# Optimization experiments

Hardware: AMD Instinct MI355X
Metric: run time of the kernel (lower is better)

The kernel has to match this reference:

```python
import jax, jax.numpy as jnp
import numpy as np

NUM_HEADS = 16


def setup_inputs() -> dict:
    key = jax.random.key(0)
    ks = jax.random.split(key, 7)
    B, S, D = 2, 2048, 1024
    scale = 1.0 / np.sqrt(D)
    return {
        "queries": jax.random.normal(ks[0], (B, S, D), jnp.float32),
        "keys": jax.random.normal(ks[1], (B, S, D), jnp.float32),
        "values": jax.random.normal(ks[2], (B, S, D), jnp.float32),
        "Wq": jax.random.normal(ks[3], (D, D), jnp.float32) * scale,
        "Wk": jax.random.normal(ks[4], (D, D), jnp.float32) * scale,
        "Wv": jax.random.normal(ks[5], (D, D), jnp.float32) * scale,
        "Wo": jax.random.normal(ks[6], (D, D), jnp.float32) * scale,
    }


def _split_heads(x, h):
    # [B, S, D] -> [B, h, S, D/h]
    B, S, D = x.shape
    return x.reshape(B, S, h, D // h).transpose(0, 2, 1, 3)


def reference(queries, keys, values, Wq, Wk, Wv, Wo):
    h = NUM_HEADS
    q = _split_heads(queries @ Wq, h)  # [B, h, S, dh]
    k = _split_heads(keys @ Wk, h)
    v = _split_heads(values @ Wv, h)
    dh = q.shape[-1]
    scores = jnp.einsum("bhqd,bhkd->bhqk", q, k) / jnp.sqrt(jnp.float32(dh))
    attn = jax.nn.softmax(scores, axis=-1)
    y = jnp.einsum("bhqk,bhkd->bhqd", attn, v)  # [B, h, S, dh]
    B, _, S, _ = y.shape
    y = y.transpose(0, 2, 1, 3).reshape(B, S, h * dh)
    return y @ Wo
```

## Files before the change

### kernel.cpp

```cpp
#include <hip/hip_runtime.h>
#include <hip/hip_bf16.h>


typedef __attribute__((ext_vector_type(8))) short bf16x8;
typedef __attribute__((ext_vector_type(4))) float f32x4;
typedef __attribute__((ext_vector_type(16))) float f32x16;
typedef __attribute__((ext_vector_type(4))) unsigned int u32x4;

#define QSCALE 0.18033688011112042f

__device__ __forceinline__ unsigned short f2b(float f) {
    unsigned int u = __float_as_uint(f);
    u += 0x7FFFu + ((u >> 16) & 1u);
    return (unsigned short)(u >> 16);
}

__device__ __forceinline__ unsigned cvt_pk_bf16(float lo, float hi) {
    unsigned r;
    asm("v_cvt_pk_bf16_f32 %0, %1, %2" : "=v"(r) : "v"(lo), "v"(hi));
    return r;
}

__device__ __forceinline__ void gld_lds16(const void* g, void* l) {
    __builtin_amdgcn_global_load_lds(
        (const __attribute__((address_space(1))) unsigned int*)g,
        (__attribute__((address_space(3))) unsigned int*)l, 16, 0, 0);
}

__global__ __launch_bounds__(256) void f32_to_bf16_3(
    const float* __restrict__ i0, const float* __restrict__ i1, const float* __restrict__ i2,
    unsigned short* __restrict__ o0, unsigned short* __restrict__ o1, unsigned short* __restrict__ o2)
{
    const int z = blockIdx.y;
    const float* in = z == 0 ? i0 : (z == 1 ? i1 : i2);
    unsigned short* out = z == 0 ? o0 : (z == 1 ? o1 : o2);
    int i = blockIdx.x * 256 + threadIdx.x;
    float4 v = ((const float4*)in)[i];
    ushort4 o;
    o.x = f2b(v.x); o.y = f2b(v.y); o.z = f2b(v.z); o.w = f2b(v.w);
    ((ushort4*)out)[i] = o;
}

__global__ __launch_bounds__(256) void transpose_w4(
    const float* __restrict__ W0, const float* __restrict__ W1,
    const float* __restrict__ W2, const float* __restrict__ W3,
    unsigned short* __restrict__ O0, unsigned short* __restrict__ O1,
    unsigned short* __restrict__ O2, unsigned short* __restrict__ O3)
{
    __shared__ unsigned short tile[32][33];
    const int z = blockIdx.z;
    const float* in = z == 0 ? W0 : z == 1 ? W1 : z == 2 ? W2 : W3;
    unsigned short* out = z == 0 ? O0 : z == 1 ? O1 : z == 2 ? O2 : O3;
    const int c0 = blockIdx.x * 32, r0 = blockIdx.y * 32;
    const int tx = threadIdx.x, ty = threadIdx.y;
#pragma unroll
    for (int i = 0; i < 4; ++i)
        tile[ty + i * 8][tx] = f2b(in[(size_t)(r0 + ty + i * 8) * 1024 + c0 + tx]);
    __syncthreads();
#pragma unroll
    for (int i = 0; i < 4; ++i)
        out[(size_t)(c0 + ty + i * 8) * 1024 + r0 + tx] = tile[tx][ty + i * 8];
}

template <int BN, int MODE>
__global__ __launch_bounds__(256) void gemm_bt(
    const unsigned short* __restrict__ A0, const unsigned short* __restrict__ A1,
    const unsigned short* __restrict__ A2,
    const unsigned short* __restrict__ B0, const unsigned short* __restrict__ B1,
    const unsigned short* __restrict__ B2,
    void* __restrict__ Cq, void* __restrict__ Ck, void* __restrict__ Cv)
{
    constexpr int K = 1024, N = 1024;
    constexpr int NB = BN / 32;
    __shared__ unsigned short lds_a[2][128 * 32];
    __shared__ unsigned short lds_b[2][BN * 32];
    const int tid = threadIdx.x;
    const int wid = tid >> 6, ln = tid & 15, lg = (tid & 63) >> 4;
    const int z = (MODE == 1) ? blockIdx.z : 0;
    const unsigned short* A = (z == 0) ? A0 : (z == 1) ? A1 : A2;
    const unsigned short* Bt = (z == 0) ? B0 : (z == 1) ? B1 : B2;
    const int m0 = blockIdx.y * 128, n0 = blockIdx.x * BN;
    const int wr = wid >> 1, wc = wid & 1;

    f32x4 acc[4][NB];
#pragma unroll
    for (int m = 0; m < 4; ++m)
#pragma unroll
        for (int n = 0; n < NB; ++n) acc[m][n] = {};

    const unsigned short* ga = A + (size_t)(m0 + (tid >> 2)) * K + (tid & 3) * 8;
    const unsigned short* gb = Bt + (size_t)(n0 + (tid >> 2)) * K + (tid & 3) * 8;

    auto stage = [&](int buf, int k0) {
        gld_lds16(ga + k0, &lds_a[buf][wid * 512]);
        gld_lds16(ga + k0 + 64 * K, &lds_a[buf][wid * 512 + 2048]);
        gld_lds16(gb + k0, &lds_b[buf][wid * 512]);
        if constexpr (BN == 128) gld_lds16(gb + k0 + 64 * K, &lds_b[buf][wid * 512 + 2048]);
    };

    stage(0, 0);
    __syncthreads();

    for (int k0 = 0; k0 < K; k0 += 32) {
        const int buf = (k0 >> 5) & 1;
        if (k0 + 32 < K) stage(buf ^ 1, k0 + 32);

        bf16x8 af[4], bfr[NB];
#pragma unroll
        for (int m = 0; m < 4; ++m)
            af[m] = *(const bf16x8*)&lds_a[buf][(wr * 64 + m * 16 + ln) * 32 + lg * 8];
#pragma unroll
        for (int n = 0; n < NB; ++n)
            bfr[n] = *(const bf16x8*)&lds_b[buf][(wc * (BN / 2) + n * 16 + ln) * 32 + lg * 8];
#pragma unroll
        for (int m = 0; m < 4; ++m)
#pragma unroll
            for (int n = 0; n < NB; ++n)
                acc[m][n] = __builtin_amdgcn_mfma_f32_16x16x32_bf16(af[m], bfr[n], acc[m][n], 0, 0, 0);
        __syncthreads();
    }

    const int gcb = n0 + wc * (BN / 2) + ln;
    const int grb = m0 + wr * 64 + lg * 4;

    if constexpr (MODE == 0) {
        float* C = (float*)Cq;
#pragma unroll
        for (int m = 0; m < 4; ++m)
#pragma unroll
            for (int n = 0; n < NB; ++n)
#pragma unroll
                for (int r = 0; r < 4; ++r)
                    C[(size_t)(grb + m * 16 + r) * N + gcb + n * 16] = acc[m][n][r];
    } else {
        if (z == 0) {
            unsigned short* C = (unsigned short*)Cq;
#pragma unroll
            for (int m = 0; m < 4; ++m)
#pragma unroll
                for (int n = 0; n < NB; ++n)
#pragma unroll
                    for (int r = 0; r < 4; ++r)
                        C[(size_t)(grb + m * 16 + r) * N + gcb + n * 16] =
                            f2b(acc[m][n][r] * QSCALE);
        } else if (z == 1) {
            unsigned short* Kp = (unsigned short*)Ck;
#pragma unroll
            for (int m = 0; m < 4; ++m)
#pragma unroll
                for (int n = 0; n < NB; ++n) {
                    int gr = grb + m * 16, gc = gcb + n * 16;
                    int bq = gr >> 11, kvg = gr & 2047, kvt = kvg >> 6;
                    int h = gc >> 6, d = gc & 63;
                    size_t img = ((size_t)(bq * 16 + h) * 32 + kvt) * 4096;
                    int ks = d >> 4, hib = (d >> 3) & 1, i = d & 7;
                    int kvb = kvg & 63, T = kvb >> 5;
                    size_t base = img + T * 2048 + ks * 512 + hib * 256 + i;
#pragma unroll
                    for (int r = 0; r < 4; ++r)
                        Kp[base + ((kvb & 31) + r) * 8] = f2b(acc[m][n][r]);
                }
        } else {
            unsigned short* Vp = (unsigned short*)Cv;
#pragma unroll
            for (int m = 0; m < 4; ++m)
#pragma unroll
                for (int n = 0; n < NB; ++n) {
                    int gr = grb + m * 16, gc = gcb + n * 16;
                    int bq = gr >> 11, kvg = gr & 2047, kvt = kvg >> 6;
                    int h = gc >> 6, d = gc & 63;
                    size_t img = ((size_t)(bq * 16 + h) * 32 + kvt) * 4096;
                    int kvb = kvg & 63;
                    int T = kvb >> 5, g = (kvb >> 3) & 3, hib = (kvb >> 2) & 1;
                    int kstep = 2 * T + (g >> 1);
                    int dt = d >> 5, ln31 = d & 31;
                    size_t addr = img + dt * 2048 + kstep * 512 + hib * 256 + ln31 * 8 + (g & 1) * 4;
                    uint2 w;
                    w.x = cvt_pk_bf16(acc[m][n][0], acc[m][n][1]);
                    w.y = cvt_pk_bf16(acc[m][n][2], acc[m][n][3]);
                    *(uint2*)(Vp + addr) = w;
                }
        }
    }
}

__global__ __launch_bounds__(128) void attn_kernel(
    const unsigned short* __restrict__ Qp,
    const unsigned short* __restrict__ Kpack,
    const unsigned short* __restrict__ Vpack,
    unsigned short* __restrict__ Y)
{
    __shared__ unsigned short lds_k[2][4096];
    __shared__ unsigned short lds_v[2][4096];
    const int tid = threadIdx.x;
    const int wid = tid >> 6, lane = tid & 63;
    const int q31 = lane & 31, hi = lane >> 5;

    const int logical = (blockIdx.x & 7) * 128 + (blockIdx.x >> 3);
    const int bx = logical & 31, bh = logical >> 5;
    const int b = bh >> 4, h = bh & 15;
    const int tok0 = b * 2048;
    const int qw = bx * 64 + wid * 32;

    const unsigned short* qrow = Qp + (size_t)(tok0 + qw + q31) * 1024 + h * 64 + hi * 8;
    bf16x8 qf[4];
#pragma unroll
    for (int ks = 0; ks < 4; ++ks) qf[ks] = *(const bf16x8*)(qrow + ks * 16);

    const unsigned short* gk = Kpack + (size_t)bh * (32 * 4096);
    const unsigned short* gv = Vpack + (size_t)bh * (32 * 4096);

    float m_run = -1e30f, l_run = 0.f;
    f32x16 o[2] = {{}, {}};

    auto stage = [&](int buf, int kvt) {
#pragma unroll
        for (int c = 0; c < 4; ++c) {
            int m = c * 2 + wid;
            gld_lds16(gk + (size_t)kvt * 4096 + m * 512 + lane * 8, &lds_k[buf][m * 512]);
            gld_lds16(gv + (size_t)kvt * 4096 + m * 512 + lane * 8, &lds_v[buf][m * 512]);
        }
    };

    stage(0, 0);
    __syncthreads();

    for (int kvt = 0; kvt < 32; ++kvt) {
        const int buf = kvt & 1;
        if (kvt < 31) stage(buf ^ 1, kvt + 1);

        f32x16 st[2];
#pragma unroll
        for (int T = 0; T < 2; ++T) {
            f32x16 zacc = {};
#pragma unroll
            for (int ks = 0; ks < 4; ++ks) {
                bf16x8 ka = *(const bf16x8*)&lds_k[buf][T * 2048 + ks * 512 + lane * 8];
                zacc = __builtin_amdgcn_mfma_f32_32x32x16_bf16(ka, qf[ks], zacc, 0, 0, 0);
            }
            st[T] = zacc;
        }

        float pm = st[0][0];
#pragma unroll
        for (int r = 1; r < 16; ++r) pm = fmaxf(pm, st[0][r]);
#pragma unroll
        for (int r = 0; r < 16; ++r) pm = fmaxf(pm, st[1][r]);
        pm = fmaxf(pm, __shfl_xor(pm, 32));
        const float mn = fmaxf(m_run, pm);
        const float alpha = __builtin_amdgcn_exp2f(m_run - mn);
        m_run = mn;

        float rs = 0.f;
        unsigned pk[2][8];
#pragma unroll
        for (int T = 0; T < 2; ++T)
#pragma unroll
            for (int g = 0; g < 4; ++g) {
                float p0 = __builtin_amdgcn_exp2f(st[T][g * 4 + 0] - mn);
                float p1 = __builtin_amdgcn_exp2f(st[T][g * 4 + 1] - mn);
                float p2 = __builtin_amdgcn_exp2f(st[T][g * 4 + 2] - mn);
                float p3 = __builtin_amdgcn_exp2f(st[T][g * 4 + 3] - mn);
                rs += (p0 + p1) + (p2 + p3);
                pk[T][g * 2 + 0] = cvt_pk_bf16(p0, p1);
                pk[T][g * 2 + 1] = cvt_pk_bf16(p2, p3);
            }
        rs += __shfl_xor(rs, 32);
        l_run = l_run * alpha + rs;

#pragma unroll
        for (int r = 0; r < 16; ++r) { o[0][r] *= alpha; o[1][r] *= alpha; }

#pragma unroll
        for (int dt = 0; dt < 2; ++dt)
#pragma unroll
            for (int kstep = 0; kstep < 4; ++kstep) {
                bf16x8 va = *(const bf16x8*)&lds_v[buf][dt * 2048 + kstep * 512 + lane * 8];
                u32x4 w = {pk[kstep >> 1][4 * (kstep & 1) + 0], pk[kstep >> 1][4 * (kstep & 1) + 1],
                           pk[kstep >> 1][4 * (kstep & 1) + 2], pk[kstep >> 1][4 * (kstep & 1) + 3]};
                o[dt] = __builtin_amdgcn_mfma_f32_32x32x16_bf16(
                    va, __builtin_bit_cast(bf16x8, w), o[dt], 0, 0, 0);
            }
        __syncthreads();
    }

    const float inv = __builtin_amdgcn_rcpf(l_run);
    unsigned short* yout = Y + (size_t)(tok0 + qw + q31) * 1024 + h * 64 + hi * 4;
#pragma unroll
    for (int dt = 0; dt < 2; ++dt)
#pragma unroll
        for (int g = 0; g < 4; ++g) {
            uint2 w;
            w.x = cvt_pk_bf16(o[dt][g * 4 + 0] * inv, o[dt][g * 4 + 1] * inv);
            w.y = cvt_pk_bf16(o[dt][g * 4 + 2] * inv, o[dt][g * 4 + 3] * inv);
            *(uint2*)(yout + dt * 32 + g * 8) = w;
        }
}

extern "C" void kernel_launch(void* const* d_in, const int* in_sizes, int n_in,
                              void* d_out, int out_size, void* d_ws, size_t ws_size,
                              hipStream_t stream)
{
    const float* q_f = (const float*)d_in[0];
    const float* k_f = (const float*)d_in[1];
    const float* v_f = (const float*)d_in[2];
    const float* Wq  = (const float*)d_in[3];
    const float* Wk  = (const float*)d_in[4];
    const float* Wv  = (const float*)d_in[5];
    const float* Wo  = (const float*)d_in[6];
    float* out = (float*)d_out;

    const size_t X = (size_t)4096 * 1024;
    const size_t W = (size_t)1024 * 1024;
    unsigned short* ws  = (unsigned short*)d_ws;
    unsigned short* qb  = ws;
    unsigned short* kb  = qb + X;
    unsigned short* vb  = kb + X;
    unsigned short* wqt = vb + X;
    unsigned short* wkt = wqt + W;
    unsigned short* wvt = wkt + W;
    unsigned short* wot = wvt + W;
    unsigned short* Qp  = wot + W;
    unsigned short* Kpk = Qp + X;
    unsigned short* Vpk = Kpk + X;
    unsigned short* Yb  = Vpk + X;

    f32_to_bf16_3<<<dim3(4096, 3), 256, 0, stream>>>(q_f, k_f, v_f, qb, kb, vb);
    transpose_w4<<<dim3(32, 32, 4), dim3(32, 8), 0, stream>>>(Wq, Wk, Wv, Wo,
                                                              wqt, wkt, wvt, wot);
    gemm_bt<128, 1><<<dim3(8, 32, 3), 256, 0, stream>>>(qb, kb, vb, wqt, wkt, wvt,
                                                        Qp, Kpk, Vpk);
    attn_kernel<<<1024, 128, 0, stream>>>(Qp, Kpk, Vpk, Yb);
    gemm_bt<64, 0><<<dim3(16, 32, 1), 256, 0, stream>>>(Yb, nullptr, nullptr,
                                                        wot, nullptr, nullptr,
                                                        out, nullptr, nullptr);
}
```

Measured before the change: 238.7 us.

## Split attention over KV halves with single-wave blocks and add combine kernel

The attention kernel now runs one 64-lane wave per block over 32 queries and half of the KV sequence, giving 4096 blocks instead of 1024. K and V fragments are read straight from global memory instead of being staged through double-buffered LDS, which removes the block barriers. A new combine kernel merges the two partial outputs using their per-row max and sum. The online softmax skips rescaling when the new max exceeds the running max by at most 8, and the max reduction is rebalanced into a tree. The trade-offs are an extra launch, extra traffic for the partial results, and uncached global loads of K and V.

Result: slower. 247.1 us (+3.5%).

```diff
diff --git a/kernel.cpp b/kernel.cpp
--- a/kernel.cpp
+++ b/kernel.cpp
@@ -13,6 +13,10 @@
     unsigned int u = __float_as_uint(f);
     u += 0x7FFFu + ((u >> 16) & 1u);
     return (unsigned short)(u >> 16);
+}
+
+__device__ __forceinline__ float b2f(unsigned short s) {
+    return __uint_as_float((unsigned int)s << 16);
 }
 
 __device__ __forceinline__ unsigned cvt_pk_bf16(float lo, float hi) {
@@ -184,50 +188,35 @@
     }
 }
 
-__global__ __launch_bounds__(128) void attn_kernel(
+__global__ __launch_bounds__(64, 4) void attn_kernel(
     const unsigned short* __restrict__ Qp,
     const unsigned short* __restrict__ Kpack,
     const unsigned short* __restrict__ Vpack,
-    unsigned short* __restrict__ Y)
-{
-    __shared__ unsigned short lds_k[2][4096];
-    __shared__ unsigned short lds_v[2][4096];
-    const int tid = threadIdx.x;
-    const int wid = tid >> 6, lane = tid & 63;
+    unsigned short* __restrict__ Opart,
+    float2* __restrict__ ML)
+{
+    const int lane = threadIdx.x;
     const int q31 = lane & 31, hi = lane >> 5;
 
-    const int logical = (blockIdx.x & 7) * 128 + (blockIdx.x >> 3);
-    const int bx = logical & 31, bh = logical >> 5;
+    const int logical = (blockIdx.x & 7) * 512 + (blockIdx.x >> 3);
+    const int qb = logical & 63, rest = logical >> 6;
+    const int bh = rest & 31, s = rest >> 5;
     const int b = bh >> 4, h = bh & 15;
-    const int tok0 = b * 2048;
-    const int qw = bx * 64 + wid * 32;
-
-    const unsigned short* qrow = Qp + (size_t)(tok0 + qw + q31) * 1024 + h * 64 + hi * 8;
+    const int q0 = qb * 32;
+
+    const unsigned short* qrow = Qp + (size_t)(b * 2048 + q0 + q31) * 1024 + h * 64 + hi * 8;
     bf16x8 qf[4];
 #pragma unroll
     for (int ks = 0; ks < 4; ++ks) qf[ks] = *(const bf16x8*)(qrow + ks * 16);
 
-    const unsigned short* gk = Kpack + (size_t)bh * (32 * 4096);
-    const unsigned short* gv = Vpack + (size_t)bh * (32 * 4096);
+    const unsigned short* gk = Kpack + (size_t)bh * (32 * 4096) + lane * 8;
+    const unsigned short* gv = Vpack + (size_t)bh * (32 * 4096) + lane * 8;
 
     float m_run = -1e30f, l_run = 0.f;
     f32x16 o[2] = {{}, {}};
 
-    auto stage = [&](int buf, int kvt) {
-#pragma unroll
-        for (int c = 0; c < 4; ++c) {
-            int m = c * 2 + wid;
-            gld_lds16(gk + (size_t)kvt * 4096 + m * 512 + lane * 8, &lds_k[buf][m * 512]);
-            gld_lds16(gv + (size_t)kvt * 4096 + m * 512 + lane * 8, &lds_v[buf][m * 512]);
-        }
-    };
-
-    stage(0, 0);
-    __syncthreads();
-
-    for (int kvt = 0; kvt < 32; ++kvt) {
-        const int buf = kvt & 1;
-        if (kvt < 31) stage(buf ^ 1, kvt + 1);
+    for (int kvt = s * 16; kvt < s * 16 + 16; ++kvt) {
+        const size_t tb = (size_t)kvt * 4096;
 
         f32x16 st[2];
 #pragma unroll
@@ -235,21 +224,42 @@
             f32x16 zacc = {};
 #pragma unroll
             for (int ks = 0; ks < 4; ++ks) {
-                bf16x8 ka = *(const bf16x8*)&lds_k[buf][T * 2048 + ks * 512 + lane * 8];
+                bf16x8 ka = *(const bf16x8*)(gk + tb + T * 2048 + ks * 512);
                 zacc = __builtin_amdgcn_mfma_f32_32x32x16_bf16(ka, qf[ks], zacc, 0, 0, 0);
             }
             st[T] = zacc;
         }
 
-        float pm = st[0][0];
-#pragma unroll
-        for (int r = 1; r < 16; ++r) pm = fmaxf(pm, st[0][r]);
-#pragma unroll
-        for (int r = 0; r < 16; ++r) pm = fmaxf(pm, st[1][r]);
+        float a0 = fmaxf(fmaxf(st[0][0], st[0][1]), st[0][2]);
+        float a1 = fmaxf(fmaxf(st[0][3], st[0][4]), st[0][5]);
+        float a2 = fmaxf(fmaxf(st[0][6], st[0][7]), st[0][8]);
+        float a3 = fmaxf(fmaxf(st[0][9], st[0][10]), st[0][11]);
+        float a4 = fmaxf(fmaxf(st[0][12], st[0][13]), st[0][14]);
+        float a5 = fmaxf(fmaxf(st[0][15], st[1][0]), st[1][1]);
+        float a6 = fmaxf(fmaxf(st[1][2], st[1][3]), st[1][4]);
+        float a7 = fmaxf(fmaxf(st[1][5], st[1][6]), st[1][7]);
+        float a8 = fmaxf(fmaxf(st[1][8], st[1][9]), st[1][10]);
+        float a9 = fmaxf(fmaxf(st[1][11], st[1][12]), st[1][13]);
+        float aa = fmaxf(st[1][14], st[1][15]);
+        a0 = fmaxf(fmaxf(a0, a1), a2);
+        a3 = fmaxf(fmaxf(a3, a4), a5);
+        a6 = fmaxf(fmaxf(a6, a7), a8);
+        a9 = fmaxf(a9, aa);
+        float pm = fmaxf(fmaxf(a0, a3), fmaxf(a6, a9));
         pm = fmaxf(pm, __shfl_xor(pm, 32));
-        const float mn = fmaxf(m_run, pm);
-        const float alpha = __builtin_amdgcn_exp2f(m_run - mn);
-        m_run = mn;
+
+        float mn;
+        bool skip = __all(pm - m_run <= 8.f);
+        if (skip) {
+            mn = m_run;
+        } else {
+            mn = fmaxf(m_run, pm);
+            const float alpha = __builtin_amdgcn_exp2f(m_run - mn);
+            m_run = mn;
+            l_run *= alpha;
+#pragma unroll
+            for (int r = 0; r < 16; ++r) { o[0][r] *= alpha; o[1][r] *= alpha; }
+        }
 
         float rs = 0.f;
         unsigned pk[2][8];
@@ -266,35 +276,63 @@
                 pk[T][g * 2 + 1] = cvt_pk_bf16(p2, p3);
             }
         rs += __shfl_xor(rs, 32);
-        l_run = l_run * alpha + rs;
-
-#pragma unroll
-        for (int r = 0; r < 16; ++r) { o[0][r] *= alpha; o[1][r] *= alpha; }
+        l_run += rs;
 
 #pragma unroll
         for (int dt = 0; dt < 2; ++dt)
 #pragma unroll
             for (int kstep = 0; kstep < 4; ++kstep) {
-                bf16x8 va = *(const bf16x8*)&lds_v[buf][dt * 2048 + kstep * 512 + lane * 8];
+                bf16x8 va = *(const bf16x8*)(gv + tb + dt * 2048 + kstep * 512);
                 u32x4 w = {pk[kstep >> 1][4 * (kstep & 1) + 0], pk[kstep >> 1][4 * (kstep & 1) + 1],
                            pk[kstep >> 1][4 * (kstep & 1) + 2], pk[kstep >> 1][4 * (kstep & 1) + 3]};
                 o[dt] = __builtin_amdgcn_mfma_f32_32x32x16_bf16(
                     va, __builtin_bit_cast(bf16x8, w), o[dt], 0, 0, 0);
             }
-        __syncthreads();
     }
 
-    const float inv = __builtin_amdgcn_rcpf(l_run);
-    unsigned short* yout = Y + (size_t)(tok0 + qw + q31) * 1024 + h * 64 + hi * 4;
+    unsigned short* op = Opart + ((size_t)(s * 32 + bh) * 2048 + q0 + q31) * 64 + hi * 4;
 #pragma unroll
     for (int dt = 0; dt < 2; ++dt)
 #pragma unroll
         for (int g = 0; g < 4; ++g) {
             uint2 w;
-            w.x = cvt_pk_bf16(o[dt][g * 4 + 0] * inv, o[dt][g * 4 + 1] * inv);
-            w.y = cvt_pk_bf16(o[dt][g * 4 + 2] * inv, o[dt][g * 4 + 3] * inv);
-            *(uint2*)(yout + dt * 32 + g * 8) = w;
+            w.x = cvt_pk_bf16(o[dt][g * 4 + 0], o[dt][g * 4 + 1]);
+            w.y = cvt_pk_bf16(o[dt][g * 4 + 2], o[dt][g * 4 + 3]);
+            *(uint2*)(op + dt * 32 + g * 8) = w;
         }
+    if (hi == 0)
+        ML[(size_t)(s * 32 + bh) * 2048 + q0 + q31] = make_float2(m_run, l_run);
+}
+
+__global__ __launch_bounds__(256) void attn_combine(
+    const unsigned short* __restrict__ Opart,
+    const float2* __restrict__ ML,
+    unsigned short* __restrict__ Y)
+{
+    const int gq = blockIdx.x * 16 + (threadIdx.x >> 4);
+    const int l16 = threadIdx.x & 15;
+    const int bh = gq >> 11, q = gq & 2047;
+    const int b = bh >> 4, h = bh & 15;
+
+    const size_t r0 = ((size_t)bh * 2048 + q) * 64 + l16 * 4;
+    const size_t r1 = ((size_t)(32 + bh) * 2048 + q) * 64 + l16 * 4;
+    ushort4 u0 = *(const ushort4*)(Opart + r0);
+    ushort4 u1 = *(const ushort4*)(Opart + r1);
+    float2 ml0 = ML[(size_t)bh * 2048 + q];
+    float2 ml1 = ML[(size_t)(32 + bh) * 2048 + q];
+
+    const float m = fmaxf(ml0.x, ml1.x);
+    float w0 = __builtin_amdgcn_exp2f(ml0.x - m);
+    float w1 = __builtin_amdgcn_exp2f(ml1.x - m);
+    const float inv = __builtin_amdgcn_rcpf(ml0.y * w0 + ml1.y * w1);
+    w0 *= inv; w1 *= inv;
+
+    uint2 w;
+    w.x = cvt_pk_bf16(b2f(u0.x) * w0 + b2f(u1.x) * w1,
+                      b2f(u0.y) * w0 + b2f(u1.y) * w1);
+    w.y = cvt_pk_bf16(b2f(u0.z) * w0 + b2f(u1.z) * w1,
+                      b2f(u0.w) * w0 + b2f(u1.w) * w1);
+    *(uint2*)(Y + (size_t)(b * 2048 + q) * 1024 + h * 64 + l16 * 4) = w;
 }
 
 extern "C" void kernel_launch(void* const* d_in, const int* in_sizes, int n_in,
@@ -324,13 +362,16 @@
     unsigned short* Kpk = Qp + X;
     unsigned short* Vpk = Kpk + X;
     unsigned short* Yb  = Vpk + X;
+    unsigned short* Opart = qb;
+    float2*         ML    = (float2*)vb;
 
     f32_to_bf16_3<<<dim3(4096, 3), 256, 0, stream>>>(q_f, k_f, v_f, qb, kb, vb);
     transpose_w4<<<dim3(32, 32, 4), dim3(32, 8), 0, stream>>>(Wq, Wk, Wv, Wo,
                                                               wqt, wkt, wvt, wot);
     gemm_bt<128, 1><<<dim3(8, 32, 3), 256, 0, stream>>>(qb, kb, vb, wqt, wkt, wvt,
                                                         Qp, Kpk, Vpk);
-    attn_kernel<<<1024, 128, 0, stream>>>(Qp, Kpk, Vpk, Yb);
+    attn_kernel<<<4096, 64, 0, stream>>>(Qp, Kpk, Vpk, Opart, ML);
+    attn_combine<<<4096, 256, 0, stream>>>(Opart, ML, Yb);
     gemm_bt<64, 0><<<dim3(16, 32, 1), 256, 0, stream>>>(Yb, nullptr, nullptr,
                                                         wot, nullptr, nullptr,
                                                         out, nullptr, nullptr);
```
